# Kernel tuning notes

Hardware: AMD Instinct MI355X
Metric: run time of the kernel (lower is better)

The kernel has to match this reference:

```python
import jax, jax.numpy as jnp
import numpy as np

DIM = 1024
HEADS = 16
DIM_HEAD = 64
NB_FEATURES = 266
EPS = 1e-4


def _gaussian_orthogonal_random_matrix(nb_rows, nb_cols, seed=0):
    # Blocks of orthogonal rows (QR of gaussian), rows rescaled by gaussian row norms (scaling=0).
    rng = np.random.default_rng(seed)
    blocks = []
    full, rem = divmod(nb_rows, nb_cols)
    for _ in range(full):
        g = rng.standard_normal((nb_cols, nb_cols))
        q, _ = np.linalg.qr(g)
        blocks.append(q.T)
    if rem > 0:
        g = rng.standard_normal((nb_cols, nb_cols))
        q, _ = np.linalg.qr(g)
        blocks.append(q.T[:rem])
    mat = np.concatenate(blocks, axis=0)
    multiplier = np.linalg.norm(rng.standard_normal((nb_rows, nb_cols)), axis=1)
    return (multiplier[:, None] * mat).astype(np.float32)


def _softmax_kernel(data, proj, is_query):
    # data: [b,h,n,d], proj: [m,d]
    d = data.shape[-1]
    data_normalizer = d ** -0.25
    ratio = proj.shape[0] ** -0.5
    data_dash = jnp.einsum('bhnd,md->bhnm', data * data_normalizer, proj)
    diag = 0.5 * (data_normalizer ** 2) * jnp.sum(data * data, axis=-1, keepdims=True)
    if is_query:
        m = jax.lax.stop_gradient(jnp.max(data_dash, axis=-1, keepdims=True))
    else:
        m = jax.lax.stop_gradient(jnp.max(data_dash, axis=(-1, -2), keepdims=True))
    return ratio * (jnp.exp(data_dash - diag - m) + EPS)


def _linear_attention(q, k, v):
    # q,k: [b,h,n,m], v: [b,h,n,e]
    k_cumsum = jnp.sum(k, axis=-2)                                   # [b,h,m]
    D_inv = 1.0 / jnp.einsum('bhnm,bhm->bhn', q, k_cumsum)           # [b,h,n]
    context = jnp.einsum('bhnm,bhne->bhme', k, v)                    # [b,h,m,e]
    return jnp.einsum('bhme,bhnm,bhn->bhne', context, q, D_inv)      # [b,h,n,e]


def setup_inputs() -> dict:
    key = jax.random.key(0)
    k1, k2, k3, k4, k5 = jax.random.split(key, 5)
    B, N = 2, 4096
    inner = HEADS * DIM_HEAD
    s = DIM ** -0.5
    return {
        'x': jax.random.normal(k1, (B, N, DIM), dtype=jnp.float32),
        'Wq': jax.random.normal(k2, (inner, DIM), dtype=jnp.float32) * s,
        'Wk': jax.random.normal(k3, (inner, DIM), dtype=jnp.float32) * s,
        'Wv': jax.random.normal(k4, (inner, DIM), dtype=jnp.float32) * s,
        'Wo': jax.random.normal(k5, (DIM, inner), dtype=jnp.float32) * s,
        'bo': jnp.zeros((DIM,), dtype=jnp.float32),
        'proj': jnp.asarray(_gaussian_orthogonal_random_matrix(NB_FEATURES, DIM_HEAD)),
    }


def reference(x, Wq, Wk, Wv, Wo, bo, proj):
    b, n, _ = x.shape
    def split_heads(t):
        return t.reshape(b, n, HEADS, DIM_HEAD).transpose(0, 2, 1, 3)  # [b,h,n,d]
    q = split_heads(x @ Wq.T)
    k = split_heads(x @ Wk.T)
    v = split_heads(x @ Wv.T)
    qp = _softmax_kernel(q, proj, is_query=True)
    kp = _softmax_kernel(k, proj, is_query=False)
    out = _linear_attention(qp, kp, v)                                # [b,h,n,d]
    out = out.transpose(0, 2, 1, 3).reshape(b, n, HEADS * DIM_HEAD)
    return out @ Wo.T + bo
```

## Files before the change

kernel.cpp:

```cpp
#include <hip/hip_runtime.h>
#include <hip/hip_bf16.h>
#include <hip/hip_fp16.h>


#define B_   2
#define N_   4096
#define H_   16
#define M_   266
#define MP_  288
#define DIM_ 1024
#define RT_  8192
#define BH_  32
#define LKN  40
#define LSB  296
#define NCH  16
#define KS_  8

typedef __attribute__((ext_vector_type(8))) short s8v;
typedef __attribute__((ext_vector_type(4))) float f4v;

__device__ __forceinline__ ushort f2bu(float x){ __hip_bfloat16 h = __float2bfloat16(x); return *(ushort*)&h; }
__device__ __forceinline__ float  bu2f(ushort u){ return __uint_as_float(((unsigned)u) << 16); }

constexpr float NORMC  = 0.35355339059327379f;
constexpr float RATIOC = 0.06131393f;
constexpr float DIAGC  = 0.0625f;
constexpr float EPSC   = 1e-4f;

__device__ __forceinline__ void stf(float* p, float v){ *p = v; }
__device__ __forceinline__ void stf(__hip_bfloat16* p, float v){ *p = __float2bfloat16(v); }

__device__ __forceinline__ void gl_lds16(const ushort* g, ushort* l){
    __builtin_amdgcn_global_load_lds(
        (const __attribute__((address_space(1))) unsigned int*)(const unsigned int*)g,
        (__attribute__((address_space(3))) unsigned int*)(unsigned int*)l,
        16, 0, 0);
}

__global__ void cast_x(const float* __restrict__ s, ushort* __restrict__ d){
    const int i = (blockIdx.x * 256 + threadIdx.x) * 8;
    const float4 a = *(const float4*)&s[i];
    const float4 b = *(const float4*)&s[i + 4];
    ushort4 lo, hi;
    lo.x = f2bu(a.x); lo.y = f2bu(a.y); lo.z = f2bu(a.z); lo.w = f2bu(a.w);
    hi.x = f2bu(b.x); hi.y = f2bu(b.y); hi.z = f2bu(b.z); hi.w = f2bu(b.w);
    *(ushort4*)&d[i]     = lo;
    *(ushort4*)&d[i + 4] = hi;
}

__global__ void cast_w(const float* s0, const float* s1, const float* s2, const float* s3,
                       ushort* d0, ushort* d1, ushort* d2, ushort* d3){
    const float* s; ushort* d;
    switch (blockIdx.y) {
        case 0: s = s0; d = d0; break;
        case 1: s = s1; d = d1; break;
        case 2: s = s2; d = d2; break;
        default: s = s3; d = d3; break;
    }
    const int i = (blockIdx.x * 256 + threadIdx.x) * 8;
    const float4 a = *(const float4*)&s[i];
    const float4 b = *(const float4*)&s[i + 4];
    ushort4 lo, hi;
    lo.x = f2bu(a.x); lo.y = f2bu(a.y); lo.z = f2bu(a.z); lo.w = f2bu(a.w);
    hi.x = f2bu(b.x); hi.y = f2bu(b.y); hi.z = f2bu(b.z); hi.w = f2bu(b.w);
    *(ushort4*)&d[i]     = lo;
    *(ushort4*)&d[i + 4] = hi;
}

__global__ void cast_proj(const float* __restrict__ p, ushort* __restrict__ pb){
    const int i = blockIdx.x * 256 + threadIdx.x;
    if (i >= MP_ * 64) return;
    const int m = i >> 6, dc = i & 63;
    pb[i] = f2bu((m < M_) ? NORMC * p[m * 64 + dc] : 0.f);
}

template<bool DIAG, bool BIAS, typename TC>
__launch_bounds__(256)
__global__ void gemm128(const ushort* __restrict__ A, const ushort* __restrict__ Bw,
                        const float* __restrict__ bias, TC* __restrict__ C,
                        float* __restrict__ diag)
{
    __shared__ ushort As[128 * 32];
    __shared__ ushort Bs[128 * 32];

    const int tid  = threadIdx.x;
    const int lane = tid & 63, wave = tid >> 6;
    const int col  = lane & 15, quad = lane >> 4;
    const int wm   = (wave & 1) * 64, wn = (wave >> 1) * 64;

    const int gX = gridDim.x, total = gX * gridDim.y, cpx = total >> 3;
    const int fl = blockIdx.x + blockIdx.y * gX;
    const int sw = (fl & 7) * cpx + (fl >> 3);
    const int r0 = (sw / gX) * 128, c0 = (sw % gX) * 128;

    const int f0 = tid * 8;
    const int row0 = f0 >> 5, kc0 = f0 & 31;
    const size_t aoff0 = (size_t)(r0 + row0) * DIM_ + kc0;
    const size_t aoff1 = (size_t)(r0 + 64 + row0) * DIM_ + kc0;
    const size_t boff0 = (size_t)(c0 + row0) * DIM_ + kc0;
    const size_t boff1 = (size_t)(c0 + 64 + row0) * DIM_ + kc0;
    ushort* asb0 = &As[wave * 512];
    ushort* asb1 = &As[2048 + wave * 512];
    ushort* bsb0 = &Bs[wave * 512];
    ushort* bsb1 = &Bs[2048 + wave * 512];

    f4v acc[4][4];
    #pragma unroll
    for (int i = 0; i < 4; ++i)
        #pragma unroll
        for (int j = 0; j < 4; ++j) acc[i][j] = (f4v){0.f, 0.f, 0.f, 0.f};

    for (int kk = 0; kk < DIM_; kk += 32) {
        gl_lds16(&A[aoff0 + kk],  asb0);
        gl_lds16(&A[aoff1 + kk],  asb1);
        gl_lds16(&Bw[boff0 + kk], bsb0);
        gl_lds16(&Bw[boff1 + kk], bsb1);
        __syncthreads();
        s8v af[4], bf[4];
        #pragma unroll
        for (int i = 0; i < 4; ++i)
            af[i] = *(const s8v*)&As[(wm + i * 16 + col) * 32 + quad * 8];
        #pragma unroll
        for (int j = 0; j < 4; ++j)
            bf[j] = *(const s8v*)&Bs[(wn + j * 16 + col) * 32 + quad * 8];
        #pragma unroll
        for (int i = 0; i < 4; ++i)
            #pragma unroll
            for (int j = 0; j < 4; ++j)
                acc[i][j] = __builtin_amdgcn_mfma_f32_16x16x32_bf16(af[i], bf[j], acc[i][j], 0, 0, 0);
        __syncthreads();
    }

    float bb[4] = {0.f, 0.f, 0.f, 0.f};
    if (BIAS) {
        #pragma unroll
        for (int j = 0; j < 4; ++j) bb[j] = bias[c0 + wn + j * 16 + col];
    }
    #pragma unroll
    for (int i = 0; i < 4; ++i) {
        #pragma unroll
        for (int r = 0; r < 4; ++r) {
            const size_t grow = (size_t)(r0 + wm + i * 16 + quad * 4 + r);
            #pragma unroll
            for (int j = 0; j < 4; ++j)
                stf(&C[grow * DIM_ + c0 + wn + j * 16 + col], acc[i][j][r] + bb[j]);
        }
    }
    if (DIAG) {
        const int hglob = (c0 + wn) >> 6;
        #pragma unroll
        for (int i = 0; i < 4; ++i) {
            #pragma unroll
            for (int r = 0; r < 4; ++r) {
                float s = 0.f;
                #pragma unroll
                for (int j = 0; j < 4; ++j) s += acc[i][j][r] * acc[i][j][r];
                s += __shfl_xor(s, 1); s += __shfl_xor(s, 2);
                s += __shfl_xor(s, 4); s += __shfl_xor(s, 8);
                if (col == 0)
                    diag[(size_t)(r0 + wm + i * 16 + quad * 4 + r) * H_ + hglob] = DIAGC * s;
            }
        }
    }
}

__launch_bounds__(256)
__global__ void gemm128_qkv(const ushort* __restrict__ A, const ushort* __restrict__ Bw,
                            ushort* __restrict__ Q, ushort* __restrict__ K,
                            ushort* __restrict__ V,
                            float* __restrict__ diagQ, float* __restrict__ diagK)
{
    __shared__ ushort As[128 * 32];
    __shared__ ushort Bs[128 * 32];

    const int tid  = threadIdx.x;
    const int lane = tid & 63, wave = tid >> 6;
    const int col  = lane & 15, quad = lane >> 4;
    const int wm   = (wave & 1) * 64, wn = (wave >> 1) * 64;

    const int fl = blockIdx.x + blockIdx.y * 24;
    const int sw = (fl & 7) * 192 + (fl >> 3);
    const int r0 = (sw / 24) * 128, c0 = (sw % 24) * 128;

    const int f0 = tid * 8;
    const int row0 = f0 >> 5, kc0 = f0 & 31;
    const size_t aoff0 = (size_t)(r0 + row0) * DIM_ + kc0;
    const size_t aoff1 = (size_t)(r0 + 64 + row0) * DIM_ + kc0;
    const size_t boff0 = (size_t)(c0 + row0) * DIM_ + kc0;
    const size_t boff1 = (size_t)(c0 + 64 + row0) * DIM_ + kc0;
    ushort* asb0 = &As[wave * 512];
    ushort* asb1 = &As[2048 + wave * 512];
    ushort* bsb0 = &Bs[wave * 512];
    ushort* bsb1 = &Bs[2048 + wave * 512];

    f4v acc[4][4];
    #pragma unroll
    for (int i = 0; i < 4; ++i)
        #pragma unroll
        for (int j = 0; j < 4; ++j) acc[i][j] = (f4v){0.f, 0.f, 0.f, 0.f};

    for (int kk = 0; kk < DIM_; kk += 32) {
        gl_lds16(&A[aoff0 + kk],  asb0);
        gl_lds16(&A[aoff1 + kk],  asb1);
        gl_lds16(&Bw[boff0 + kk], bsb0);
        gl_lds16(&Bw[boff1 + kk], bsb1);
        __syncthreads();
        s8v af[4], bf[4];
        #pragma unroll
        for (int i = 0; i < 4; ++i)
            af[i] = *(const s8v*)&As[(wm + i * 16 + col) * 32 + quad * 8];
        #pragma unroll
        for (int j = 0; j < 4; ++j)
            bf[j] = *(const s8v*)&Bs[(wn + j * 16 + col) * 32 + quad * 8];
        #pragma unroll
        for (int i = 0; i < 4; ++i)
            #pragma unroll
            for (int j = 0; j < 4; ++j)
                acc[i][j] = __builtin_amdgcn_mfma_f32_16x16x32_bf16(af[i], bf[j], acc[i][j], 0, 0, 0);
        __syncthreads();
    }

    const int which = c0 >> 10;
    const int cc    = c0 & 1023;
    ushort* C = (which == 0) ? Q : ((which == 1) ? K : V);
    float* dptr = (which == 0) ? diagQ : ((which == 1) ? diagK : nullptr);

    #pragma unroll
    for (int i = 0; i < 4; ++i) {
        #pragma unroll
        for (int r = 0; r < 4; ++r) {
            const size_t grow = (size_t)(r0 + wm + i * 16 + quad * 4 + r);
            #pragma unroll
            for (int j = 0; j < 4; ++j)
                C[grow * DIM_ + cc + wn + j * 16 + col] = f2bu(acc[i][j][r]);
        }
    }
    if (dptr) {
        const int hglob = (cc + wn) >> 6;
        #pragma unroll
        for (int i = 0; i < 4; ++i) {
            #pragma unroll
            for (int r = 0; r < 4; ++r) {
                float s = 0.f;
                #pragma unroll
                for (int j = 0; j < 4; ++j) s += acc[i][j][r] * acc[i][j][r];
                s += __shfl_xor(s, 1); s += __shfl_xor(s, 2);
                s += __shfl_xor(s, 4); s += __shfl_xor(s, 8);
                if (col == 0)
                    dptr[(size_t)(r0 + wm + i * 16 + quad * 4 + r) * H_ + hglob] = DIAGC * s;
            }
        }
    }
}

__launch_bounds__(256)
__global__ void kctx_mfma(const ushort* __restrict__ Kb, const ushort* __restrict__ Vb,
                          const ushort* __restrict__ projb,
                          const float* __restrict__ diagK,
                          float* __restrict__ ctxp, float* __restrict__ kcsp,
                          float* __restrict__ vsump, float* __restrict__ kmaxp)
{
    __shared__ ushort Pl[MP_ * 64];
    __shared__ ushort Kp[MP_ * LKN];
    __shared__ ushort Vt[64 * LKN];
    __shared__ float kred[2][MP_];
    __shared__ float wmx[4];

    const int tid  = threadIdx.x;
    const int lane = tid & 63, wave = tid >> 6;
    const int col  = lane & 15, quad = lane >> 4;
    const int bh   = blockIdx.y, b = bh >> 4, h = bh & 15;
    const int n0   = blockIdx.x * (N_ / NCH);
    const int rowblk = wave >> 1;
    const int t0 = (wave & 1) * 9;

    for (int i = tid; i < MP_ * 8; i += 256) {
        const int m = i >> 3, c = i & 7;
        *(uint4*)&Pl[m * 64 + ((c ^ (m & 7)) << 3)] = *(const uint4*)&projb[m * 64 + (c << 3)];
    }
    const int sw0 = (quad ^ (col & 7)) << 3;
    const int sw1 = ((quad | 4) ^ (col & 7)) << 3;
    __syncthreads();

    float mx = -3.4e38f;
    {
        size_t arA = ((size_t)(b * N_ + n0 + rowblk * 16 + col)) * DIM_ + h * 64 + quad * 8;
        s8v pA0 = *(const s8v*)&Kb[arA];
        s8v pA1 = *(const s8v*)&Kb[arA + 32];
        for (int ks = 0; ks < KS_; ++ks) {
            const s8v a0 = pA0, a1 = pA1;
            if (ks + 1 < KS_) {
                arA += (size_t)32 * DIM_;
                pA0 = *(const s8v*)&Kb[arA];
                pA1 = *(const s8v*)&Kb[arA + 32];
            }
            for (int t = t0; t < t0 + 9; ++t) {
                const s8v bf0 = *(const s8v*)&Pl[(t * 16 + col) * 64 + sw0];
                const s8v bf1 = *(const s8v*)&Pl[(t * 16 + col) * 64 + sw1];
                f4v a = (f4v){0.f, 0.f, 0.f, 0.f};
                a = __builtin_amdgcn_mfma_f32_16x16x32_bf16(a0, bf0, a, 0, 0, 0);
                a = __builtin_amdgcn_mfma_f32_16x16x32_bf16(a1, bf1, a, 0, 0, 0);
                if (t * 16 + col < M_) {
                    #pragma unroll
                    for (int r = 0; r < 4; ++r) mx = fmaxf(mx, a[r]);
                }
            }
        }
    }
    #pragma unroll
    for (int o = 32; o > 0; o >>= 1) mx = fmaxf(mx, __shfl_xor(mx, o));
    if (lane == 0) wmx[wave] = mx;
    __syncthreads();
    const float mc = fmaxf(fmaxf(wmx[0], wmx[1]), fmaxf(wmx[2], wmx[3]));
    if (tid == 0) kmaxp[bh * NCH + blockIdx.x] = mc;

    const int nst = tid & 31, est = (tid >> 5) * 8;
    s8v vvP = *(const s8v*)&Vb[((size_t)(b * N_ + n0 + nst)) * DIM_ + h * 64 + est];
    const size_t arow0 = ((size_t)(b * N_ + n0 + rowblk * 16 + col)) * DIM_ + h * 64 + quad * 8;
    s8v afP0 = *(const s8v*)&Kb[arow0];
    s8v afP1 = *(const s8v*)&Kb[arow0 + 32];
    float dgrP[4];
    #pragma unroll
    for (int r = 0; r < 4; ++r)
        dgrP[r] = diagK[((size_t)(b * N_ + n0 + rowblk * 16 + quad * 4 + r)) * H_ + h];

    f4v facc[18];
    #pragma unroll
    for (int t = 0; t < 18; ++t) facc[t] = (f4v){0.f, 0.f, 0.f, 0.f};
    float kcsa[9] = {};
    float vsa[8] = {};

    for (int ks = 0; ks < KS_; ++ks) {
        const s8v vv = vvP, af0 = afP0, af1 = afP1;
        float dgr[4];
        #pragma unroll
        for (int r = 0; r < 4; ++r) dgr[r] = dgrP[r];

        #pragma unroll
        for (int j = 0; j < 8; ++j) {
            const ushort uv = ((const ushort*)&vv)[j];
            Vt[(est + j) * LKN + nst] = uv;
            vsa[j] += bu2f(uv);
        }

        for (int t = t0; t < t0 + 9; ++t) {
            const s8v bf0 = *(const s8v*)&Pl[(t * 16 + col) * 64 + sw0];
            const s8v bf1 = *(const s8v*)&Pl[(t * 16 + col) * 64 + sw1];
            f4v a = (f4v){0.f, 0.f, 0.f, 0.f};
            a = __builtin_amdgcn_mfma_f32_16x16x32_bf16(af0, bf0, a, 0, 0, 0);
            a = __builtin_amdgcn_mfma_f32_16x16x32_bf16(af1, bf1, a, 0, 0, 0);
            const int m = t * 16 + col;
            float kp[4];
            #pragma unroll
            for (int r = 0; r < 4; ++r) {
                float v = 0.f;
                if (m < M_) v = __expf(a[r] - dgr[r] - mc);
                kp[r] = v;
            }
            kcsa[t - t0] += kp[0] + kp[1] + kp[2] + kp[3];
            ushort4 pk;
            pk.x = f2bu(kp[0]); pk.y = f2bu(kp[1]); pk.z = f2bu(kp[2]); pk.w = f2bu(kp[3]);
            *(ushort4*)&Kp[m * LKN + rowblk * 16 + quad * 4] = pk;
        }

        if (ks + 1 < KS_) {
            const int nb1 = n0 + (ks + 1) * 32;
            vvP  = *(const s8v*)&Vb[((size_t)(b * N_ + nb1 + nst)) * DIM_ + h * 64 + est];
            const size_t arow1 = ((size_t)(b * N_ + nb1 + rowblk * 16 + col)) * DIM_ + h * 64 + quad * 8;
            afP0 = *(const s8v*)&Kb[arow1];
            afP1 = *(const s8v*)&Kb[arow1 + 32];
            #pragma unroll
            for (int r = 0; r < 4; ++r)
                dgrP[r] = diagK[((size_t)(b * N_ + nb1 + rowblk * 16 + quad * 4 + r)) * H_ + h];
        }
        __syncthreads();
        const s8v bfe = *(const s8v*)&Vt[(wave * 16 + col) * LKN + quad * 8];
        #pragma unroll
        for (int t = 0; t < 18; ++t) {
            const s8v am = *(const s8v*)&Kp[(t * 16 + col) * LKN + quad * 8];
            facc[t] = __builtin_amdgcn_mfma_f32_16x16x32_bf16(am, bfe, facc[t], 0, 0, 0);
        }
        __syncthreads();
    }

    const size_t pbase = ((size_t)bh * NCH + blockIdx.x) * (MP_ * 64);
    #pragma unroll
    for (int t = 0; t < 18; ++t) {
        #pragma unroll
        for (int r = 0; r < 4; ++r)
            ctxp[pbase + (size_t)(t * 16 + quad * 4 + r) * 64 + wave * 16 + col] = facc[t][r];
    }
    #pragma unroll
    for (int j = 0; j < 8; ++j) {
        float s = vsa[j];
        s += __shfl_xor(s, 1);  s += __shfl_xor(s, 2);
        s += __shfl_xor(s, 4);  s += __shfl_xor(s, 8);
        s += __shfl_xor(s, 16);
        if ((lane & 31) == 0)
            vsump[((size_t)bh * NCH + blockIdx.x) * 64 + est + j] = s;
    }
    for (int t = t0; t < t0 + 9; ++t) {
        float s = kcsa[t - t0];
        s += __shfl_xor(s, 16);
        s += __shfl_xor(s, 32);
        if (quad == 0) kred[rowblk][t * 16 + col] = s;
    }
    __syncthreads();
    for (int i = tid; i < MP_; i += 256)
        kcsp[((size_t)bh * NCH + blockIdx.x) * MP_ + i] = kred[0][i] + kred[1][i];
}

__launch_bounds__(256)
__global__ void ctx_reduce(const float* __restrict__ ctxp, const float* __restrict__ kcsp,
                           const float* __restrict__ vsump, const float* __restrict__ kmaxp,
                           ushort* __restrict__ ctxT, float* __restrict__ kcs)
{
    __shared__ float scl[NCH];
    __shared__ float vsl[64];
    const int bh = blockIdx.y, tid = threadIdx.x;

    if (tid < NCH) {
        float M = -3.4e38f;
        #pragma unroll
        for (int c = 0; c < NCH; ++c) M = fmaxf(M, kmaxp[bh * NCH + c]);
        scl[tid] = __expf(kmaxp[bh * NCH + tid] - M);
    }
    if (tid >= 64 && tid < 128) {
        const int e = tid - 64;
        float s = 0.f;
        #pragma unroll
        for (int c = 0; c < NCH; ++c) s += vsump[((size_t)bh * NCH + c) * 64 + e];
        vsl[e] = s;
    }
    __syncthreads();

    const int base = blockIdx.x * (MP_ * 64 / 8);
    const size_t cb = (size_t)bh * NCH * (MP_ * 64);
    #pragma unroll
    for (int u = 0; u < 9; ++u) {
        const int flat = base + u * 256 + tid;
        float s = 0.f;
        #pragma unroll
        for (int c = 0; c < NCH; ++c) s += scl[c] * ctxp[cb + (size_t)c * (MP_ * 64) + flat];
        const int m = flat >> 6, e = flat & 63;
        ctxT[((size_t)bh * 64 + e) * MP_ + m] = f2bu(RATIOC * (s + EPSC * vsl[e]));
    }
    if (blockIdx.x == 0) {
        for (int i = tid; i < MP_; i += 256) {
            float s = 0.f;
            #pragma unroll
            for (int c = 0; c < NCH; ++c) s += scl[c] * kcsp[((size_t)bh * NCH + c) * MP_ + i];
            kcs[(size_t)bh * MP_ + i] = RATIOC * (s + EPSC * (float)N_);
        }
    }
}

__launch_bounds__(256)
__global__ void qdashout(const ushort* __restrict__ Qb, const ushort* __restrict__ projb,
                         const float* __restrict__ diagQ, const float* __restrict__ kcs,
                         const ushort* __restrict__ ctxT, ushort* __restrict__ Ab)
{
    __shared__ ushort SB[64 * LSB];
    __shared__ float kcl[MP_];
    __shared__ float dinv[64];

    const int tid  = threadIdx.x;
    const int lane = tid & 63, wave = tid >> 6;
    const int col  = lane & 15, quad = lane >> 4;
    const int bh   = blockIdx.y, b = bh >> 4, h = bh & 15;
    const int n0   = blockIdx.x * 64;

    const size_t arow = ((size_t)(b * N_ + n0 + wave * 16 + col)) * DIM_ + h * 64 + quad * 8;
    const s8v af0 = *(const s8v*)&Qb[arow];
    const s8v af1 = *(const s8v*)&Qb[arow + 32];
    float dgr[4];
    #pragma unroll
    for (int r = 0; r < 4; ++r)
        dgr[r] = diagQ[((size_t)(b * N_ + n0 + wave * 16 + quad * 4 + r)) * H_ + h];

    for (int i = tid; i < MP_ * 8; i += 256) {
        const int m = i >> 3, c = i & 7;
        *(uint4*)&SB[m * 64 + ((c ^ (m & 7)) << 3)] = *(const uint4*)&projb[m * 64 + (c << 3)];
    }
    for (int i = tid; i < MP_; i += 256) kcl[i] = kcs[(size_t)bh * MP_ + i];
    __syncthreads();

    const int sw0 = (quad ^ (col & 7)) << 3;
    const int sw1 = ((quad | 4) ^ (col & 7)) << 3;

    f4v acc[17];
    #pragma unroll
    for (int t = 0; t < 17; ++t) {
        const s8v bf0 = *(const s8v*)&SB[(t * 16 + col) * 64 + sw0];
        const s8v bf1 = *(const s8v*)&SB[(t * 16 + col) * 64 + sw1];
        f4v a = (f4v){0.f, 0.f, 0.f, 0.f};
        a = __builtin_amdgcn_mfma_f32_16x16x32_bf16(af0, bf0, a, 0, 0, 0);
        a = __builtin_amdgcn_mfma_f32_16x16x32_bf16(af1, bf1, a, 0, 0, 0);
        acc[t] = a;
    }

    float rmx[4];
    #pragma unroll
    for (int r = 0; r < 4; ++r) {
        float mx = -3.4e38f;
        #pragma unroll
        for (int t = 0; t < 16; ++t) mx = fmaxf(mx, acc[t][r]);
        if (col < 10) mx = fmaxf(mx, acc[16][r]);
        mx = fmaxf(mx, __shfl_xor(mx, 1));
        mx = fmaxf(mx, __shfl_xor(mx, 2));
        mx = fmaxf(mx, __shfl_xor(mx, 4));
        mx = fmaxf(mx, __shfl_xor(mx, 8));
        rmx[r] = mx;
    }

    float den[4] = {0.f, 0.f, 0.f, 0.f};
    #pragma unroll
    for (int t = 0; t < 17; ++t) {
        const int m = t * 16 + col;
        const float kc = kcl[m];
        #pragma unroll
        for (int r = 0; r < 4; ++r) {
            float v = 0.f;
            if (m < M_)
                v = RATIOC * (__expf(acc[t][r] - dgr[r] - rmx[r]) + EPSC);
            acc[t][r] = v;
            den[r] += v * kc;
        }
    }

    const ushort* ct = ctxT + (size_t)bh * 64 * MP_;
    s8v bfA[4], bfB[4];
    #pragma unroll
    for (int j = 0; j < 4; ++j)
        bfA[j] = *(const s8v*)&ct[(size_t)(j * 16 + col) * MP_ + quad * 8];

    __syncthreads();

    #pragma unroll
    for (int r = 0; r < 4; ++r) {
        const int rb = (wave * 16 + quad * 4 + r) * LSB;
        #pragma unroll
        for (int t = 0; t < 17; ++t)
            SB[rb + t * 16 + col] = f2bu(acc[t][r]);
        if (col < 8) *(uint*)&SB[rb + 272 + col * 2] = 0u;
    }
    #pragma unroll
    for (int r = 0; r < 4; ++r) {
        float d = den[r];
        d += __shfl_xor(d, 1); d += __shfl_xor(d, 2);
        d += __shfl_xor(d, 4); d += __shfl_xor(d, 8);
        if (col == 0)
            dinv[wave * 16 + quad * 4 + r] = 1.0f / fmaxf(d, 1e-30f);
    }
    __syncthreads();

    f4v acc2[4];
    #pragma unroll
    for (int j = 0; j < 4; ++j) acc2[j] = (f4v){0.f, 0.f, 0.f, 0.f};
    #pragma unroll
    for (int kp = 0; kp < 4; ++kp) {
        const int k0 = 2 * kp, k1 = 2 * kp + 1, k2 = 2 * kp + 2;
        #pragma unroll
        for (int j = 0; j < 4; ++j)
            bfB[j] = *(const s8v*)&ct[(size_t)(j * 16 + col) * MP_ + k1 * 32 + quad * 8];
        const s8v afrA = *(const s8v*)&SB[(wave * 16 + col) * LSB + k0 * 32 + quad * 8];
        #pragma unroll
        for (int j = 0; j < 4; ++j)
            acc2[j] = __builtin_amdgcn_mfma_f32_16x16x32_bf16(afrA, bfA[j], acc2[j], 0, 0, 0);
        #pragma unroll
        for (int j = 0; j < 4; ++j)
            bfA[j] = *(const s8v*)&ct[(size_t)(j * 16 + col) * MP_ + k2 * 32 + quad * 8];
        const s8v afrB = *(const s8v*)&SB[(wave * 16 + col) * LSB + k1 * 32 + quad * 8];
        #pragma unroll
        for (int j = 0; j < 4; ++j)
            acc2[j] = __builtin_amdgcn_mfma_f32_16x16x32_bf16(afrB, bfB[j], acc2[j], 0, 0, 0);
    }
    {
        const s8v afrT = *(const s8v*)&SB[(wave * 16 + col) * LSB + 8 * 32 + quad * 8];
        #pragma unroll
        for (int j = 0; j < 4; ++j)
            acc2[j] = __builtin_amdgcn_mfma_f32_16x16x32_bf16(afrT, bfA[j], acc2[j], 0, 0, 0);
    }
    #pragma unroll
    for (int j = 0; j < 4; ++j) {
        #pragma unroll
        for (int r = 0; r < 4; ++r) {
            const int n = wave * 16 + quad * 4 + r;
            Ab[((size_t)(b * N_ + n0 + n)) * DIM_ + h * 64 + j * 16 + col] =
                f2bu(acc2[j][r] * dinv[n]);
        }
    }
}

extern "C" void kernel_launch(void* const* d_in, const int* in_sizes, int n_in,
                              void* d_out, int out_size, void* d_ws, size_t ws_size,
                              hipStream_t stream)
{
    const float* x    = (const float*)d_in[0];
    const float* Wq   = (const float*)d_in[1];
    const float* Wk   = (const float*)d_in[2];
    const float* Wv   = (const float*)d_in[3];
    const float* Wo   = (const float*)d_in[4];
    const float* bo   = (const float*)d_in[5];
    const float* proj = (const float*)d_in[6];

    char* ws = (char*)d_ws;
    size_t o = 0;
    ushort* xb    = (ushort*)(ws + o); o += (size_t)RT_ * DIM_ * 2;
    ushort* Wqb   = (ushort*)(ws + o); o += (size_t)DIM_ * DIM_ * 2;
    ushort* Wkb   = (ushort*)(ws + o); o += (size_t)DIM_ * DIM_ * 2;
    ushort* Wvb   = (ushort*)(ws + o); o += (size_t)DIM_ * DIM_ * 2;
    ushort* Wob   = (ushort*)(ws + o); o += (size_t)DIM_ * DIM_ * 2;
    ushort* projb = (ushort*)(ws + o); o += (size_t)MP_ * 64 * 2;
    ushort* Qb    = (ushort*)(ws + o); o += (size_t)RT_ * DIM_ * 2;
    ushort* Kb    = (ushort*)(ws + o); o += (size_t)RT_ * DIM_ * 2;
    ushort* Vb    = (ushort*)(ws + o); o += (size_t)RT_ * DIM_ * 2;
    ushort* Ab    = (ushort*)(ws + o); o += (size_t)RT_ * DIM_ * 2;
    float*    ctxp  = (float*)(ws + o);    o += (size_t)BH_ * NCH * MP_ * 64 * 4;
    float*    kcsp  = (float*)(ws + o);    o += (size_t)BH_ * NCH * MP_ * 4;
    float*    kcs   = (float*)(ws + o);    o += (size_t)BH_ * MP_ * 4;
    float*    vsump = (float*)(ws + o);    o += (size_t)BH_ * NCH * 64 * 4;
    float*    kmaxp = (float*)(ws + o);    o += (size_t)BH_ * NCH * 4;
    float*    diagQ = (float*)(ws + o);    o += (size_t)RT_ * H_ * 4;
    float*    diagK = (float*)(ws + o);    o += (size_t)RT_ * H_ * 4;
    ushort*   ctxT  = (ushort*)(ws + o);   o += (size_t)BH_ * 64 * MP_ * 2;

    cast_x<<<dim3(RT_ * DIM_ / 2048), 256, 0, stream>>>(x, xb);
    cast_w<<<dim3(DIM_ * DIM_ / 2048, 4), 256, 0, stream>>>(Wq, Wk, Wv, Wo, Wqb, Wkb, Wvb, Wob);
    cast_proj<<<dim3(MP_ * 64 / 256), 256, 0, stream>>>(proj, projb);

    gemm128_qkv<<<dim3(24, RT_ / 128), 256, 0, stream>>>(xb, Wqb, Qb, Kb, Vb, diagQ, diagK);

    kctx_mfma<<<dim3(NCH, BH_), 256, 0, stream>>>(Kb, Vb, projb, diagK, ctxp, kcsp, vsump, kmaxp);
    ctx_reduce<<<dim3(8, BH_), 256, 0, stream>>>(ctxp, kcsp, vsump, kmaxp, ctxT, kcs);
    qdashout<<<dim3(N_ / 64, BH_), 256, 0, stream>>>(Qb, projb, diagQ, kcs, ctxT, Ab);

    gemm128<false, true, float><<<dim3(DIM_ / 128, RT_ / 128), 256, 0, stream>>>(Ab, Wob, bo, (float*)d_out, nullptr);
}
```

Baseline: 278.5 us.

## Rewrite QKV GEMM as 256x256 tile with 4-stage LDS ring pipeline

```diff
diff --git a/kernel.cpp b/kernel.cpp
--- a/kernel.cpp
+++ b/kernel.cpp
@@ -37,6 +37,11 @@
         16, 0, 0);
 }
 
+#define WAITVM(N) asm volatile("s_waitcnt vmcnt(" #N ")" ::: "memory")
+#define SBAR()    __builtin_amdgcn_s_barrier()
+#define CFENCE()  asm volatile("" ::: "memory")
+#define SCHEDB()  __builtin_amdgcn_sched_barrier(0)
+
 __global__ void cast_x(const float* __restrict__ s, ushort* __restrict__ d){
     const int i = (blockIdx.x * 256 + threadIdx.x) * 8;
     const float4 a = *(const float4*)&s[i];
@@ -164,90 +169,98 @@
     }
 }
 
-__launch_bounds__(256)
-__global__ void gemm128_qkv(const ushort* __restrict__ A, const ushort* __restrict__ Bw,
+__launch_bounds__(512, 2)
+__global__ void gemm256_qkv(const ushort* __restrict__ A, const ushort* __restrict__ Bw,
                             ushort* __restrict__ Q, ushort* __restrict__ K,
                             ushort* __restrict__ V,
                             float* __restrict__ diagQ, float* __restrict__ diagK)
 {
-    __shared__ ushort As[128 * 32];
-    __shared__ ushort Bs[128 * 32];
+    __shared__ ushort ring[65536];
 
     const int tid  = threadIdx.x;
-    const int lane = tid & 63, wave = tid >> 6;
-    const int col  = lane & 15, quad = lane >> 4;
-    const int wm   = (wave & 1) * 64, wn = (wave >> 1) * 64;
-
-    const int fl = blockIdx.x + blockIdx.y * 24;
-    const int sw = (fl & 7) * 192 + (fl >> 3);
-    const int r0 = (sw / 24) * 128, c0 = (sw % 24) * 128;
-
-    const int f0 = tid * 8;
-    const int row0 = f0 >> 5, kc0 = f0 & 31;
-    const size_t aoff0 = (size_t)(r0 + row0) * DIM_ + kc0;
-    const size_t aoff1 = (size_t)(r0 + 64 + row0) * DIM_ + kc0;
-    const size_t boff0 = (size_t)(c0 + row0) * DIM_ + kc0;
-    const size_t boff1 = (size_t)(c0 + 64 + row0) * DIM_ + kc0;
-    ushort* asb0 = &As[wave * 512];
-    ushort* asb1 = &As[2048 + wave * 512];
-    ushort* bsb0 = &Bs[wave * 512];
-    ushort* bsb1 = &Bs[2048 + wave * 512];
-
-    f4v acc[4][4];
-    #pragma unroll
-    for (int i = 0; i < 4; ++i)
-        #pragma unroll
-        for (int j = 0; j < 4; ++j) acc[i][j] = (f4v){0.f, 0.f, 0.f, 0.f};
-
-    for (int kk = 0; kk < DIM_; kk += 32) {
-        gl_lds16(&A[aoff0 + kk],  asb0);
-        gl_lds16(&A[aoff1 + kk],  asb1);
-        gl_lds16(&Bw[boff0 + kk], bsb0);
-        gl_lds16(&Bw[boff1 + kk], bsb1);
-        __syncthreads();
-        s8v af[4], bf[4];
-        #pragma unroll
-        for (int i = 0; i < 4; ++i)
-            af[i] = *(const s8v*)&As[(wm + i * 16 + col) * 32 + quad * 8];
-        #pragma unroll
-        for (int j = 0; j < 4; ++j)
-            bf[j] = *(const s8v*)&Bs[(wn + j * 16 + col) * 32 + quad * 8];
-        #pragma unroll
-        for (int i = 0; i < 4; ++i)
-            #pragma unroll
-            for (int j = 0; j < 4; ++j)
-                acc[i][j] = __builtin_amdgcn_mfma_f32_16x16x32_bf16(af[i], bf[j], acc[i][j], 0, 0, 0);
-        __syncthreads();
-    }
-
-    const int which = c0 >> 10;
-    const int cc    = c0 & 1023;
+    const int ln   = tid & 63, wv = tid >> 6;
+    const int col  = ln & 15, quad = ln >> 4;
+    const int wm   = wv >> 2, wn = wv & 3;
+
+    const int fl = blockIdx.x + blockIdx.y * 12;
+    const int sw = (fl & 7) * 48 + (fl >> 3);
+    const int r0 = (sw / 12) * 256, c0 = (sw % 12) * 256;
+
+    const int srow = wv * 16 + (ln >> 2);
+    const int lb   = ((ln & 3) - (ln >> 3)) & 3;
+    const ushort* gA0 = &A [(size_t)(r0 + srow) * DIM_ + lb * 8];
+    const ushort* gA1 = gA0 + (size_t)128 * DIM_;
+    const ushort* gB0 = &Bw[(size_t)(c0 + srow) * DIM_ + lb * 8];
+    const ushort* gB1 = gB0 + (size_t)128 * DIM_;
+    const int ldso = wv * 512;
+
+    const int rc = col * 32 + (((quad + (col >> 1)) & 3) * 8);
+
+    f4v acc[8][4];
+    #pragma unroll
+    for (int mf = 0; mf < 8; ++mf)
+        #pragma unroll
+        for (int nf = 0; nf < 4; ++nf) acc[mf][nf] = (f4v){0.f, 0.f, 0.f, 0.f};
+
+    #define QKV_STG(T) { const int so_ = ((T) & 3) * 16384; const int ko_ = (T) * 32; \
+        gl_lds16(gA0 + ko_, &ring[so_ + ldso]); \
+        gl_lds16(gA1 + ko_, &ring[so_ + 4096  + ldso]); \
+        gl_lds16(gB0 + ko_, &ring[so_ + 8192  + ldso]); \
+        gl_lds16(gB1 + ko_, &ring[so_ + 12288 + ldso]); }
+
+    #define QKV_CMP(SO) { \
+        const int soA_ = (SO) + wm * 4096 + rc; \
+        const int soB_ = (SO) + 8192 + wn * 2048 + rc; \
+        s8v af[8], bf[4]; \
+        af[0] = *(const s8v*)&ring[soA_];        af[1] = *(const s8v*)&ring[soA_ + 512]; \
+        af[2] = *(const s8v*)&ring[soA_ + 1024]; af[3] = *(const s8v*)&ring[soA_ + 1536]; \
+        af[4] = *(const s8v*)&ring[soA_ + 2048]; af[5] = *(const s8v*)&ring[soA_ + 2560]; \
+        af[6] = *(const s8v*)&ring[soA_ + 3072]; af[7] = *(const s8v*)&ring[soA_ + 3584]; \
+        bf[0] = *(const s8v*)&ring[soB_];        bf[1] = *(const s8v*)&ring[soB_ + 512]; \
+        bf[2] = *(const s8v*)&ring[soB_ + 1024]; bf[3] = *(const s8v*)&ring[soB_ + 1536]; \
+        __builtin_amdgcn_s_setprio(1); \
+        _Pragma("unroll") \
+        for (int mf_ = 0; mf_ < 8; ++mf_) \
+            _Pragma("unroll") \
+            for (int nf_ = 0; nf_ < 4; ++nf_) \
+                acc[mf_][nf_] = __builtin_amdgcn_mfma_f32_16x16x32_bf16(af[mf_], bf[nf_], acc[mf_][nf_], 0, 0, 0); \
+        __builtin_amdgcn_s_setprio(0); }
+
+    QKV_STG(0); QKV_STG(1); QKV_STG(2);
+
+    for (int t = 0; t < 29; ++t) {
+        QKV_STG(t + 3);
+        WAITVM(12); SBAR(); SCHEDB();
+        QKV_CMP((t & 3) * 16384);
+        CFENCE(); SCHEDB(); SBAR();
+    }
+    WAITVM(8); SBAR(); SCHEDB(); QKV_CMP(1 * 16384); CFENCE(); SCHEDB(); SBAR();
+    WAITVM(4); SBAR(); SCHEDB(); QKV_CMP(2 * 16384); CFENCE(); SCHEDB(); SBAR();
+    WAITVM(0); SBAR(); SCHEDB(); QKV_CMP(3 * 16384);
+    #undef QKV_STG
+    #undef QKV_CMP
+
+    const int cg = c0 + wn * 64;
+    const int which = cg >> 10, cc = cg & 1023;
     ushort* C = (which == 0) ? Q : ((which == 1) ? K : V);
     float* dptr = (which == 0) ? diagQ : ((which == 1) ? diagK : nullptr);
-
-    #pragma unroll
-    for (int i = 0; i < 4; ++i) {
+    const int hglob = cc >> 6;
+
+    #pragma unroll
+    for (int mf = 0; mf < 8; ++mf) {
         #pragma unroll
         for (int r = 0; r < 4; ++r) {
-            const size_t grow = (size_t)(r0 + wm + i * 16 + quad * 4 + r);
+            const size_t grow = (size_t)(r0 + wm * 128 + mf * 16 + quad * 4 + r);
             #pragma unroll
-            for (int j = 0; j < 4; ++j)
-                C[grow * DIM_ + cc + wn + j * 16 + col] = f2bu(acc[i][j][r]);
-        }
-    }
-    if (dptr) {
-        const int hglob = (cc + wn) >> 6;
-        #pragma unroll
-        for (int i = 0; i < 4; ++i) {
-            #pragma unroll
-            for (int r = 0; r < 4; ++r) {
+            for (int nf = 0; nf < 4; ++nf)
+                C[grow * DIM_ + cc + nf * 16 + col] = f2bu(acc[mf][nf][r]);
+            if (dptr) {
                 float s = 0.f;
                 #pragma unroll
-                for (int j = 0; j < 4; ++j) s += acc[i][j][r] * acc[i][j][r];
+                for (int nf = 0; nf < 4; ++nf) s += acc[mf][nf][r] * acc[mf][nf][r];
                 s += __shfl_xor(s, 1); s += __shfl_xor(s, 2);
                 s += __shfl_xor(s, 4); s += __shfl_xor(s, 8);
-                if (col == 0)
-                    dptr[(size_t)(r0 + wm + i * 16 + quad * 4 + r) * H_ + hglob] = DIAGC * s;
+                if (col == 0) dptr[grow * H_ + hglob] = DIAGC * s;
             }
         }
     }
@@ -629,7 +642,7 @@
     cast_w<<<dim3(DIM_ * DIM_ / 2048, 4), 256, 0, stream>>>(Wq, Wk, Wv, Wo, Wqb, Wkb, Wvb, Wob);
     cast_proj<<<dim3(MP_ * 64 / 256), 256, 0, stream>>>(proj, projb);
 
-    gemm128_qkv<<<dim3(24, RT_ / 128), 256, 0, stream>>>(xb, Wqb, Qb, Kb, Vb, diagQ, diagK);
+    gemm256_qkv<<<dim3(12, RT_ / 256), 512, 0, stream>>>(xb, Wqb, Qb, Kb, Vb, diagQ, diagK);
 
     kctx_mfma<<<dim3(NCH, BH_), 256, 0, stream>>>(Kb, Vb, projb, diagK, ctxp, kcsp, vsump, kmaxp);
     ctx_reduce<<<dim3(8, BH_), 256, 0, stream>>>(ctxp, kcsp, vsump, kmaxp, ctxT, kcs);
```

New measurement: 285.2 us. 2.4% more time.

## Double K-tile depth in QKV GEMM and swizzle LDS layout

Applied to the files above, without the earlier changes.

```diff
diff --git a/kernel.cpp b/kernel.cpp
--- a/kernel.cpp
+++ b/kernel.cpp
@@ -170,8 +170,8 @@
                             ushort* __restrict__ V,
                             float* __restrict__ diagQ, float* __restrict__ diagK)
 {
-    __shared__ ushort As[128 * 32];
-    __shared__ ushort Bs[128 * 32];
+    __shared__ ushort As[128 * 64];
+    __shared__ ushort Bs[128 * 64];
 
     const int tid  = threadIdx.x;
     const int lane = tid & 63, wave = tid >> 6;
@@ -182,16 +182,12 @@
     const int sw = (fl & 7) * 192 + (fl >> 3);
     const int r0 = (sw / 24) * 128, c0 = (sw % 24) * 128;
 
-    const int f0 = tid * 8;
-    const int row0 = f0 >> 5, kc0 = f0 & 31;
-    const size_t aoff0 = (size_t)(r0 + row0) * DIM_ + kc0;
-    const size_t aoff1 = (size_t)(r0 + 64 + row0) * DIM_ + kc0;
-    const size_t boff0 = (size_t)(c0 + row0) * DIM_ + kc0;
-    const size_t boff1 = (size_t)(c0 + 64 + row0) * DIM_ + kc0;
-    ushort* asb0 = &As[wave * 512];
-    ushort* asb1 = &As[2048 + wave * 512];
-    ushort* bsb0 = &Bs[wave * 512];
-    ushort* bsb1 = &Bs[2048 + wave * 512];
+    const int lb = ((lane & 7) - (lane >> 3)) & 7;
+    const size_t abase = (size_t)(r0 + wave * 8 + (lane >> 3)) * DIM_ + lb * 8;
+    const size_t bbase = (size_t)(c0 + wave * 8 + (lane >> 3)) * DIM_ + lb * 8;
+
+    const int rs0 = ((0 + quad + (col & 7)) & 7) * 8;
+    const int rs1 = ((4 + quad + (col & 7)) & 7) * 8;
 
     f4v acc[4][4];
     #pragma unroll
@@ -199,24 +195,41 @@
         #pragma unroll
         for (int j = 0; j < 4; ++j) acc[i][j] = (f4v){0.f, 0.f, 0.f, 0.f};
 
-    for (int kk = 0; kk < DIM_; kk += 32) {
-        gl_lds16(&A[aoff0 + kk],  asb0);
-        gl_lds16(&A[aoff1 + kk],  asb1);
-        gl_lds16(&Bw[boff0 + kk], bsb0);
-        gl_lds16(&Bw[boff1 + kk], bsb1);
+    for (int kk = 0; kk < DIM_; kk += 64) {
+        #pragma unroll
+        for (int c = 0; c < 4; ++c) {
+            gl_lds16(&A[abase  + (size_t)c * 32 * DIM_ + kk], &As[c * 2048 + wave * 512]);
+            gl_lds16(&Bw[bbase + (size_t)c * 32 * DIM_ + kk], &Bs[c * 2048 + wave * 512]);
+        }
         __syncthreads();
-        s8v af[4], bf[4];
-        #pragma unroll
-        for (int i = 0; i < 4; ++i)
-            af[i] = *(const s8v*)&As[(wm + i * 16 + col) * 32 + quad * 8];
-        #pragma unroll
-        for (int j = 0; j < 4; ++j)
-            bf[j] = *(const s8v*)&Bs[(wn + j * 16 + col) * 32 + quad * 8];
-        #pragma unroll
-        for (int i = 0; i < 4; ++i)
+        {
+            s8v af[4], bf[4];
+            #pragma unroll
+            for (int i = 0; i < 4; ++i)
+                af[i] = *(const s8v*)&As[(wm + i * 16 + col) * 64 + rs0];
             #pragma unroll
             for (int j = 0; j < 4; ++j)
-                acc[i][j] = __builtin_amdgcn_mfma_f32_16x16x32_bf16(af[i], bf[j], acc[i][j], 0, 0, 0);
+                bf[j] = *(const s8v*)&Bs[(wn + j * 16 + col) * 64 + rs0];
+            #pragma unroll
+            for (int i = 0; i < 4; ++i)
+                #pragma unroll
+                for (int j = 0; j < 4; ++j)
+                    acc[i][j] = __builtin_amdgcn_mfma_f32_16x16x32_bf16(af[i], bf[j], acc[i][j], 0, 0, 0);
+        }
+        {
+            s8v af[4], bf[4];
+            #pragma unroll
+            for (int i = 0; i < 4; ++i)
+                af[i] = *(const s8v*)&As[(wm + i * 16 + col) * 64 + rs1];
+            #pragma unroll
+            for (int j = 0; j < 4; ++j)
+                bf[j] = *(const s8v*)&Bs[(wn + j * 16 + col) * 64 + rs1];
+            #pragma unroll
+            for (int i = 0; i < 4; ++i)
+                #pragma unroll
+                for (int j = 0; j < 4; ++j)
+                    acc[i][j] = __builtin_amdgcn_mfma_f32_16x16x32_bf16(af[i], bf[j], acc[i][j], 0, 0, 0);
+        }
         __syncthreads();
     }
 
```

New measurement: 278.7 us. About the same (+0.1%).
